# Kernel tuning notes

Hardware: AMD Instinct MI355X
Metric: run time of the kernel (lower is better)

The kernel has to match this reference:

```python
import jax, jax.numpy as jnp
import numpy as np

N, E, F, H, C1 = 50000, 1_600_000, 48, 1, 16  # nodes, edges, in_feats, heads, conv out


def setup_inputs() -> dict:
    key = jax.random.key(0)
    ks = jax.random.split(key, 12)
    in_ = jax.random.normal(ks[0], (N, F), dtype=jnp.float32)
    edge_index = jax.random.randint(ks[1], (2, E), 0, N, dtype=jnp.int64)
    labels = jax.random.bernoulli(ks[2], 0.5, (N, 1)).astype(jnp.float32)
    weights = jax.random.uniform(ks[3], (N, 1), dtype=jnp.float32) + 0.5
    s = 0.1  # PyG FeaStConv init: normal(0, 0.1)
    W = jax.random.normal(ks[4], (F, H * C1), dtype=jnp.float32) * s
    u = jax.random.normal(ks[5], (F, H), dtype=jnp.float32) * s
    c = jax.random.normal(ks[6], (H,), dtype=jnp.float32) * s
    bias = jax.random.normal(ks[7], (C1,), dtype=jnp.float32) * s
    lin1_w = jax.random.normal(ks[8], (C1, 8), dtype=jnp.float32) * (1.0 / np.sqrt(C1))
    lin1_b = jnp.zeros((8,), dtype=jnp.float32)
    out_w = jax.random.normal(ks[9], (8, 1), dtype=jnp.float32) * (1.0 / np.sqrt(8))
    out_b = jnp.zeros((1,), dtype=jnp.float32)
    return {"in_": in_, "edge_index": edge_index, "labels": labels,
            "weights": weights, "W": W, "u": u, "c": c, "bias": bias,
            "lin1_w": lin1_w, "lin1_b": lin1_b, "out_w": out_w, "out_b": out_b}


def feast_conv(x, edge_index, W, u, c, bias):
    n = x.shape[0]
    loop = jnp.arange(n, dtype=edge_index.dtype)  # add_self_loops=True
    src = jnp.concatenate([edge_index[0], loop])
    dst = jnp.concatenate([edge_index[1], loop])
    xj = x[src]                                   # [E+N, F] gather
    xi = x[dst]
    q = jax.nn.softmax((xj - xi) @ u + c, axis=-1)            # [E+N, H]
    xw = (xj @ W).reshape(-1, H, C1)                           # [E+N, H, C1]
    msg = jnp.einsum('ehc,eh->ec', xw, q)                      # [E+N, C1]
    agg = jax.ops.segment_sum(msg, dst, num_segments=n)        # scatter-sum
    deg = jax.ops.segment_sum(jnp.ones_like(dst, dtype=x.dtype), dst, num_segments=n)
    return agg / jnp.maximum(deg, 1.0)[:, None] + bias         # mean aggregation


def reference(in_, edge_index, labels, weights, W, u, c, bias, lin1_w, lin1_b, out_w, out_b):
    x = jax.nn.relu(feast_conv(in_, edge_index, W, u, c, bias))
    x = jax.nn.relu(x @ lin1_w + lin1_b)
    p = jax.nn.sigmoid(x @ out_w + out_b)                      # [N, 1]
    eps = 1e-7
    pc = jnp.clip(p, eps, 1.0 - eps)
    bce = -(labels * jnp.log(pc) + (1.0 - labels) * jnp.log(1.0 - pc))
    loss = jnp.mean(weights * bce)
    return (loss, p)
```

## Files before the change

kernel.cpp:

```cpp
#include <hip/hip_runtime.h>

constexpr int N_NODES  = 50000;
constexpr int N_EDGES  = 1600000;
constexpr int F_IN     = 48;
constexpr int C1_OUT   = 16;

constexpr int BNODES    = 64;
constexpr int NBINS     = 782;
constexpr int FILL_BLKS = 256;
constexpr int EPB       = N_EDGES / FILL_BLKS;
constexpr int SCAP      = 16;
constexpr int OCAP      = 16384;
constexpr int BIN_INTS  = FILL_BLKS * SCAP;
constexpr int ROWCAP    = 98;
constexpr int XW_BLKS   = 49;

constexpr size_t OCNT_OFF  = 0;
constexpr size_t OFLOW_OFF = 256;
constexpr size_t PART_OFF  = OFLOW_OFF + (size_t)OCAP * 4;
constexpr size_t XW_OFF    = PART_OFF + 4096;
constexpr size_t GSLOT_OFF = XW_OFF + (size_t)N_NODES * C1_OUT * 4;

__device__ __forceinline__ void xw_body(int n, const float* __restrict__ x,
                                        const float* __restrict__ W,
                                        float* __restrict__ xw)
{
    const float4* xr = (const float4*)(x + (long)n * F_IN);
    float h[C1_OUT];
    #pragma unroll
    for (int c = 0; c < C1_OUT; ++c) h[c] = 0.f;
    #pragma unroll
    for (int k = 0; k < F_IN / 4; ++k) {
        float4 v = xr[k];
        #pragma unroll
        for (int c = 0; c < C1_OUT; ++c) {
            h[c] = fmaf(v.x, W[(4*k+0)*C1_OUT + c],
                   fmaf(v.y, W[(4*k+1)*C1_OUT + c],
                   fmaf(v.z, W[(4*k+2)*C1_OUT + c],
                   fmaf(v.w, W[(4*k+3)*C1_OUT + c], h[c]))));
        }
    }
    float4* o = (float4*)(xw + (long)n * C1_OUT);
    o[0] = make_float4(h[0],  h[1],  h[2],  h[3]);
    o[1] = make_float4(h[4],  h[5],  h[6],  h[7]);
    o[2] = make_float4(h[8],  h[9],  h[10], h[11]);
    o[3] = make_float4(h[12], h[13], h[14], h[15]);
}

__global__ __launch_bounds__(1024)
void k_fill_xw(const int* __restrict__ src, const int* __restrict__ dst,
               int* __restrict__ gslot, int* __restrict__ ocnt,
               unsigned int* __restrict__ oflow,
               const float* __restrict__ x, const float* __restrict__ W,
               float* __restrict__ xw)
{
    __shared__ int lcnt[NBINS];
    __shared__ int lstage[NBINS * SCAP];

    if (blockIdx.x >= FILL_BLKS) {
        int n = (blockIdx.x - FILL_BLKS) * 1024 + threadIdx.x;
        if (n < N_NODES) xw_body(n, x, W, xw);
        return;
    }

    int tid = threadIdx.x;
    if (tid < NBINS) lcnt[tid] = 0;
    __syncthreads();

    int e0 = blockIdx.x * EPB;
    for (int i = tid; i < EPB; i += 1024) {
        int e = e0 + i;
        int s = src[e], d = dst[e];
        int b = d >> 6;
        int p = atomicAdd(&lcnt[b], 1);
        if (p < SCAP) {
            lstage[(b << 4) + p] = (s << 6) | (d & 63);
        } else {
            int g = atomicAdd(ocnt, 1);
            if (g < OCAP) oflow[g] = ((unsigned)s << 16) | (unsigned)d;
        }
    }
    __syncthreads();

    for (int idx = tid; idx < NBINS * SCAP; idx += 1024) {
        int b = idx >> 4, s = idx & 15;
        int v = (s < lcnt[b]) ? lstage[idx] : -1;
        gslot[((size_t)b * FILL_BLKS + blockIdx.x) * SCAP + s] = v;
    }
}

__global__ __launch_bounds__(256)
void k_agg(const int* __restrict__ gslot, const int* __restrict__ ocnt,
           const unsigned int* __restrict__ oflow, const float* __restrict__ xw,
           const float* __restrict__ bias, const float* __restrict__ lin1_w,
           const float* __restrict__ lin1_b, const float* __restrict__ out_w,
           const float* __restrict__ out_b, const float* __restrict__ labels,
           const float* __restrict__ weights, float* __restrict__ out,
           float* __restrict__ partials)
{
    __shared__ int ndeg[BNODES];
    __shared__ unsigned short lrow[BNODES][ROWCAP];
    __shared__ float acc[BNODES][17];
    __shared__ float sLossW[4];

    int B = blockIdx.x, tid = threadIdx.x, lane = tid & 63, w = tid >> 6;

    if (tid < BNODES) ndeg[tid] = 0;
    __syncthreads();

    const int4* sp = (const int4*)(gslot + (size_t)B * BIN_INTS);
    int4 q0 = sp[tid], q1 = sp[tid + 256], q2 = sp[tid + 512], q3 = sp[tid + 768];

    int oc = *ocnt; if (oc > OCAP) oc = OCAP;

    #define SC1(v) if ((v) >= 0) { int ln = (v) & 63;               \
        int p = atomicAdd(&ndeg[ln], 1);                            \
        if (p < ROWCAP) lrow[ln][p] = (unsigned short)((unsigned)(v) >> 6); }
    SC1(q0.x); SC1(q0.y); SC1(q0.z); SC1(q0.w);
    SC1(q1.x); SC1(q1.y); SC1(q1.z); SC1(q1.w);
    SC1(q2.x); SC1(q2.y); SC1(q2.z); SC1(q2.w);
    SC1(q3.x); SC1(q3.y); SC1(q3.z); SC1(q3.w);
    #undef SC1
    for (int i = tid; i < oc; i += 256) {
        unsigned v = oflow[i];
        int d = (int)(v & 0xffffu);
        if ((d >> 6) == B) {
            int ln = d & 63;
            int p = atomicAdd(&ndeg[ln], 1);
            if (p < ROWCAP) lrow[ln][p] = (unsigned short)(v >> 16);
        }
    }
    __syncthreads();

    int rslot = lane >> 2, c4 = lane & 3;
    #pragma unroll
    for (int i = 0; i < 16; i += 2) {
        int ln0 = w * 16 + i, ln1 = ln0 + 1;
        int d0 = ndeg[ln0]; if (d0 > ROWCAP) d0 = ROWCAP;
        int d1 = ndeg[ln1]; if (d1 > ROWCAP) d1 = ROWCAP;
        int m = (d0 > d1) ? d0 : d1;
        float4 a0 = make_float4(0.f, 0.f, 0.f, 0.f);
        float4 a1 = make_float4(0.f, 0.f, 0.f, 0.f);
        for (int j0 = 0; j0 < m; j0 += 16) {
            int j = j0 + rslot;
            if (j < d0) {
                int s = lrow[ln0][j];
                float4 v = ((const float4*)(xw + (size_t)s * C1_OUT))[c4];
                a0.x += v.x; a0.y += v.y; a0.z += v.z; a0.w += v.w;
            }
            if (j < d1) {
                int s = lrow[ln1][j];
                float4 v = ((const float4*)(xw + (size_t)s * C1_OUT))[c4];
                a1.x += v.x; a1.y += v.y; a1.z += v.z; a1.w += v.w;
            }
        }
        #pragma unroll
        for (int off = 4; off < 64; off <<= 1) {
            a0.x += __shfl_xor(a0.x, off, 64);
            a1.x += __shfl_xor(a1.x, off, 64);
            a0.y += __shfl_xor(a0.y, off, 64);
            a1.y += __shfl_xor(a1.y, off, 64);
            a0.z += __shfl_xor(a0.z, off, 64);
            a1.z += __shfl_xor(a1.z, off, 64);
            a0.w += __shfl_xor(a0.w, off, 64);
            a1.w += __shfl_xor(a1.w, off, 64);
        }
        if (lane < 8) {
            int ln = (lane < 4) ? ln0 : ln1;
            float4 a = (lane < 4) ? a0 : a1;
            int c = lane & 3;
            acc[ln][c * 4 + 0] = a.x;
            acc[ln][c * 4 + 1] = a.y;
            acc[ln][c * 4 + 2] = a.z;
            acc[ln][c * 4 + 3] = a.w;
        }
    }

    float lossw = 0.f;
    if (lane < 16) {
        int ln = w * 16 + lane;
        int n = B * BNODES + ln;
        if (n < N_NODES) {
            int dg = ndeg[ln]; if (dg > ROWCAP) dg = ROWCAP;
            float inv = 1.f / (float)(dg + 1);
            const float4* xs4 = (const float4*)(xw + (size_t)n * C1_OUT);
            float xs[16];
            ((float4*)xs)[0] = xs4[0]; ((float4*)xs)[1] = xs4[1];
            ((float4*)xs)[2] = xs4[2]; ((float4*)xs)[3] = xs4[3];
            float h[16];
            #pragma unroll
            for (int c = 0; c < 16; ++c)
                h[c] = fmaxf(fmaf(acc[ln][c] + xs[c], inv, bias[c]), 0.f);
            float z = out_b[0];
            #pragma unroll
            for (int j = 0; j < 8; ++j) {
                float t = lin1_b[j];
                #pragma unroll
                for (int k = 0; k < 16; ++k) t = fmaf(h[k], lin1_w[k * 8 + j], t);
                z = fmaf(fmaxf(t, 0.f), out_w[j], z);
            }
            float p = 1.f / (1.f + __expf(-z));
            out[1 + n] = p;
            const float eps = 1e-7f;
            float pc = fminf(fmaxf(p, eps), 1.f - eps);
            float y  = labels[n];
            lossw = weights[n] * (-(y * __logf(pc) + (1.f - y) * __logf(1.f - pc)));
        }
    }
    lossw += __shfl_xor(lossw, 1, 64);
    lossw += __shfl_xor(lossw, 2, 64);
    lossw += __shfl_xor(lossw, 4, 64);
    lossw += __shfl_xor(lossw, 8, 64);
    if (lane == 0) sLossW[w] = lossw;
    __syncthreads();
    if (tid == 0)
        partials[B] = sLossW[0] + sLossW[1] + sLossW[2] + sLossW[3];
}

__global__ __launch_bounds__(1024)
void k_loss_final(const float* __restrict__ partials, float* __restrict__ out)
{
    __shared__ float sw[16];
    int tid = threadIdx.x, lane = tid & 63, wv = tid >> 6;
    float s = (tid < NBINS) ? partials[tid] : 0.f;
    #pragma unroll
    for (int off = 32; off > 0; off >>= 1) s += __shfl_down(s, off, 64);
    if (lane == 0) sw[wv] = s;
    __syncthreads();
    if (tid == 0) {
        float t = 0.f;
        #pragma unroll
        for (int k = 0; k < 16; ++k) t += sw[k];
        out[0] = t / (float)N_NODES;
    }
}

extern "C" void kernel_launch(void* const* d_in, const int* in_sizes, int n_in,
                              void* d_out, int out_size, void* d_ws, size_t ws_size,
                              hipStream_t stream)
{
    const float* x       = (const float*)d_in[0];
    const int*   eidx    = (const int*)  d_in[1];
    const float* labels  = (const float*)d_in[2];
    const float* weights = (const float*)d_in[3];
    const float* W       = (const float*)d_in[4];
    const float* bias    = (const float*)d_in[7];
    const float* lin1_w  = (const float*)d_in[8];
    const float* lin1_b  = (const float*)d_in[9];
    const float* out_w   = (const float*)d_in[10];
    const float* out_b   = (const float*)d_in[11];
    float* out = (float*)d_out;

    const int* src = eidx;
    const int* dst = eidx + N_EDGES;
    char* ws = (char*)d_ws;

    int*          ocnt     = (int*)(ws + OCNT_OFF);
    unsigned int* oflow    = (unsigned int*)(ws + OFLOW_OFF);
    float*        partials = (float*)(ws + PART_OFF);
    float*        xw       = (float*)(ws + XW_OFF);
    int*          gslot    = (int*)(ws + GSLOT_OFF);

    hipMemsetAsync(ocnt, 0, sizeof(int), stream);
    k_fill_xw<<<FILL_BLKS + XW_BLKS, 1024, 0, stream>>>(
        src, dst, gslot, ocnt, oflow, x, W, xw);
    k_agg<<<NBINS, 256, 0, stream>>>(
        gslot, ocnt, oflow, xw, bias, lin1_w, lin1_b,
        out_w, out_b, labels, weights, out, partials);
    k_loss_final<<<1, 1024, 0, stream>>>(partials, out);
}
```

Before: 138.1 us.

## Fuse final loss reduction into aggregation kernel and double block size

Removes the separate single-block loss-reduction kernel. Each aggregation block now atomically adds its partial loss to a global accumulator, and the last block to arrive (found through an atomic counter) writes the mean. The aggregation kernel also moves from 256 to 512 threads per block, so each wave handles 8 nodes instead of 16 and each thread loads fewer slot vectors. This saves one kernel launch and adds more parallelism per bin, but float atomics make the loss summation order nondeterministic.

```diff
diff --git a/kernel.cpp b/kernel.cpp
--- a/kernel.cpp
+++ b/kernel.cpp
@@ -15,10 +15,8 @@
 constexpr int ROWCAP    = 98;
 constexpr int XW_BLKS   = 49;
 
-constexpr size_t OCNT_OFF  = 0;
 constexpr size_t OFLOW_OFF = 256;
-constexpr size_t PART_OFF  = OFLOW_OFF + (size_t)OCAP * 4;
-constexpr size_t XW_OFF    = PART_OFF + 4096;
+constexpr size_t XW_OFF    = OFLOW_OFF + (size_t)OCAP * 4;
 constexpr size_t GSLOT_OFF = XW_OFF + (size_t)N_NODES * C1_OUT * 4;
 
 __device__ __forceinline__ void xw_body(int n, const float* __restrict__ x,
@@ -89,19 +87,18 @@
     }
 }
 
-__global__ __launch_bounds__(256)
-void k_agg(const int* __restrict__ gslot, const int* __restrict__ ocnt,
+__global__ __launch_bounds__(512)
+void k_agg(const int* __restrict__ gslot, int* __restrict__ ctrl,
            const unsigned int* __restrict__ oflow, const float* __restrict__ xw,
            const float* __restrict__ bias, const float* __restrict__ lin1_w,
            const float* __restrict__ lin1_b, const float* __restrict__ out_w,
            const float* __restrict__ out_b, const float* __restrict__ labels,
-           const float* __restrict__ weights, float* __restrict__ out,
-           float* __restrict__ partials)
+           const float* __restrict__ weights, float* __restrict__ out)
 {
     __shared__ int ndeg[BNODES];
     __shared__ unsigned short lrow[BNODES][ROWCAP];
     __shared__ float acc[BNODES][17];
-    __shared__ float sLossW[4];
+    __shared__ float sLossW[8];
 
     int B = blockIdx.x, tid = threadIdx.x, lane = tid & 63, w = tid >> 6;
 
@@ -109,19 +106,17 @@
     __syncthreads();
 
     const int4* sp = (const int4*)(gslot + (size_t)B * BIN_INTS);
-    int4 q0 = sp[tid], q1 = sp[tid + 256], q2 = sp[tid + 512], q3 = sp[tid + 768];
-
-    int oc = *ocnt; if (oc > OCAP) oc = OCAP;
+    int4 q0 = sp[tid], q1 = sp[tid + 512];
+
+    int oc = ctrl[0]; if (oc > OCAP) oc = OCAP;
 
     #define SC1(v) if ((v) >= 0) { int ln = (v) & 63;               \
         int p = atomicAdd(&ndeg[ln], 1);                            \
         if (p < ROWCAP) lrow[ln][p] = (unsigned short)((unsigned)(v) >> 6); }
     SC1(q0.x); SC1(q0.y); SC1(q0.z); SC1(q0.w);
     SC1(q1.x); SC1(q1.y); SC1(q1.z); SC1(q1.w);
-    SC1(q2.x); SC1(q2.y); SC1(q2.z); SC1(q2.w);
-    SC1(q3.x); SC1(q3.y); SC1(q3.z); SC1(q3.w);
     #undef SC1
-    for (int i = tid; i < oc; i += 256) {
+    for (int i = tid; i < oc; i += 512) {
         unsigned v = oflow[i];
         int d = (int)(v & 0xffffu);
         if ((d >> 6) == B) {
@@ -134,8 +129,8 @@
 
     int rslot = lane >> 2, c4 = lane & 3;
     #pragma unroll
-    for (int i = 0; i < 16; i += 2) {
-        int ln0 = w * 16 + i, ln1 = ln0 + 1;
+    for (int i = 0; i < 8; i += 2) {
+        int ln0 = w * 8 + i, ln1 = ln0 + 1;
         int d0 = ndeg[ln0]; if (d0 > ROWCAP) d0 = ROWCAP;
         int d1 = ndeg[ln1]; if (d1 > ROWCAP) d1 = ROWCAP;
         int m = (d0 > d1) ? d0 : d1;
@@ -177,8 +172,8 @@
     }
 
     float lossw = 0.f;
-    if (lane < 16) {
-        int ln = w * 16 + lane;
+    if (lane < 8) {
+        int ln = w * 8 + lane;
         int n = B * BNODES + ln;
         if (n < N_NODES) {
             int dg = ndeg[ln]; if (dg > ROWCAP) dg = ROWCAP;
@@ -210,28 +205,21 @@
     lossw += __shfl_xor(lossw, 1, 64);
     lossw += __shfl_xor(lossw, 2, 64);
     lossw += __shfl_xor(lossw, 4, 64);
-    lossw += __shfl_xor(lossw, 8, 64);
     if (lane == 0) sLossW[w] = lossw;
     __syncthreads();
-    if (tid == 0)
-        partials[B] = sLossW[0] + sLossW[1] + sLossW[2] + sLossW[3];
-}
-
-__global__ __launch_bounds__(1024)
-void k_loss_final(const float* __restrict__ partials, float* __restrict__ out)
-{
-    __shared__ float sw[16];
-    int tid = threadIdx.x, lane = tid & 63, wv = tid >> 6;
-    float s = (tid < NBINS) ? partials[tid] : 0.f;
-    #pragma unroll
-    for (int off = 32; off > 0; off >>= 1) s += __shfl_down(s, off, 64);
-    if (lane == 0) sw[wv] = s;
-    __syncthreads();
+
     if (tid == 0) {
         float t = 0.f;
         #pragma unroll
-        for (int k = 0; k < 16; ++k) t += sw[k];
-        out[0] = t / (float)N_NODES;
+        for (int k = 0; k < 8; ++k) t += sLossW[k];
+        float* loss_acc = (float*)&ctrl[2];
+        atomicAdd(loss_acc, t);
+        __threadfence();
+        int r = atomicAdd(&ctrl[1], 1);
+        if (r == NBINS - 1) {
+            float total = atomicAdd(loss_acc, 0.f);
+            out[0] = total / (float)N_NODES;
+        }
     }
 }
 
@@ -255,17 +243,15 @@
     const int* dst = eidx + N_EDGES;
     char* ws = (char*)d_ws;
 
-    int*          ocnt     = (int*)(ws + OCNT_OFF);
-    unsigned int* oflow    = (unsigned int*)(ws + OFLOW_OFF);
-    float*        partials = (float*)(ws + PART_OFF);
-    float*        xw       = (float*)(ws + XW_OFF);
-    int*          gslot    = (int*)(ws + GSLOT_OFF);
-
-    hipMemsetAsync(ocnt, 0, sizeof(int), stream);
+    int*          ctrl  = (int*)ws;
+    unsigned int* oflow = (unsigned int*)(ws + OFLOW_OFF);
+    float*        xw    = (float*)(ws + XW_OFF);
+    int*          gslot = (int*)(ws + GSLOT_OFF);
+
+    hipMemsetAsync(ctrl, 0, 12, stream);
     k_fill_xw<<<FILL_BLKS + XW_BLKS, 1024, 0, stream>>>(
-        src, dst, gslot, ocnt, oflow, x, W, xw);
-    k_agg<<<NBINS, 256, 0, stream>>>(
-        gslot, ocnt, oflow, xw, bias, lin1_w, lin1_b,
-        out_w, out_b, labels, weights, out, partials);
-    k_loss_final<<<1, 1024, 0, stream>>>(partials, out);
-}
+        src, dst, gslot, ctrl, oflow, x, W, xw);
+    k_agg<<<NBINS, 512, 0, stream>>>(
+        gslot, ctrl, oflow, xw, bias, lin1_w, lin1_b,
+        out_w, out_b, labels, weights, out);
+}
```

New measurement: 155.9 us. +12.9%, slower.
